# Optimization experiments

Measured on AMD Instinct MI355X. Metric: run time of the kernel, lower is better.

Reference implementation:

```python
import jax, jax.numpy as jnp
import numpy as np

N_HEAD = 16
N_EMBD = 1024
D_HEAD = N_EMBD // N_HEAD


def setup_inputs() -> dict:
    key = jax.random.key(0)
    ks = jax.random.split(key, 5)
    B, T, C = 4, 2048, N_EMBD
    s = 1.0 / np.sqrt(C)
    return {
        "x": jax.random.normal(ks[0], (B, T, C), dtype=jnp.float32),
        "w_qkv": jax.random.normal(ks[1], (C, 3 * C), dtype=jnp.float32) * s,
        "b_qkv": jnp.zeros((3 * C,), dtype=jnp.float32),
        "w_out": jax.random.normal(ks[2], (C, C), dtype=jnp.float32) * s,
        "b_out": jnp.zeros((C,), dtype=jnp.float32),
    }


def reference(x, w_qkv, b_qkv, w_out, b_out):
    B, T, C = x.shape
    qkv = x @ w_qkv + b_qkv  # [B,T,3C]
    q, k, v = jnp.split(qkv, 3, axis=-1)
    # [B,T,C] -> [B,H,T,D]
    def heads(t):
        return t.reshape(B, T, N_HEAD, D_HEAD).transpose(0, 2, 1, 3)
    q, k, v = heads(q), heads(k), heads(v)
    scores = jnp.einsum("bhqd,bhkd->bhqk", q, k) / np.sqrt(D_HEAD)
    causal = jnp.tril(jnp.ones((T, T), dtype=bool))
    scores = jnp.where(causal, scores, -jnp.inf)
    probs = jax.nn.softmax(scores, axis=-1)
    out = jnp.einsum("bhqk,bhkd->bhqd", probs, v)  # [B,H,T,D]
    out = out.transpose(0, 2, 1, 3).reshape(B, T, C)
    return out @ w_out + b_out
```

## Files before the change

### kernel.cpp

```cpp
#include <hip/hip_runtime.h>
#include <hip/hip_bf16.h>
#include <cstdint>
#include <cstddef>

typedef __attribute__((ext_vector_type(8))) short short8;
typedef __attribute__((ext_vector_type(4))) float f32x4;
typedef __attribute__((ext_vector_type(4))) uint16_t ushort4_t;

__device__ __forceinline__ uint16_t f2bf(float f) {
  union { float f; uint32_t u; } v; v.f = f;
  uint32_t r = v.u + 0x7FFFu + ((v.u >> 16) & 1u);
  return (uint16_t)(r >> 16);
}

__device__ __forceinline__ uint16_t f2bf_hw(float f) {
  union { __hip_bfloat16 h; uint16_t u; } cv;
  cv.h = __float2bfloat16(f);
  return cv.u;
}


__global__ __launch_bounds__(256) void cvt_f32_bf16(const float* __restrict__ in,
                                                    uint16_t* __restrict__ out, int n4) {
  int i = blockIdx.x * 256 + threadIdx.x;
  int stride = gridDim.x * 256;
  for (; i < n4; i += stride) {
    float4 v = ((const float4*)in)[i];
    ushort4_t o = { f2bf(v.x), f2bf(v.y), f2bf(v.z), f2bf(v.w) };
    ((ushort4_t*)out)[i] = o;
  }
}

__global__ __launch_bounds__(256) void transpose_cvt(const float* __restrict__ in,
                                                     uint16_t* __restrict__ out, int R, int C) {
  __shared__ float tile[32][33];
  int c0 = blockIdx.x * 32, r0 = blockIdx.y * 32;
  int tx = threadIdx.x, ty = threadIdx.y;
#pragma unroll
  for (int j = 0; j < 32; j += 8)
    tile[ty + j][tx] = in[(size_t)(r0 + ty + j) * C + c0 + tx];
  __syncthreads();
#pragma unroll
  for (int j = 0; j < 32; j += 8)
    out[(size_t)(c0 + ty + j) * R + r0 + tx] = f2bf(tile[tx][ty + j]);
}

__global__ __launch_bounds__(256) void transpose_v(const uint16_t* __restrict__ in,
                                                   uint16_t* __restrict__ out) {
  __shared__ uint16_t tile[32][33];
  int bh = blockIdx.z;
  int t0 = blockIdx.x * 32, d0 = blockIdx.y * 32;
  const uint16_t* ip = in + (size_t)bh * 2048 * 64;
  uint16_t* op = out + (size_t)bh * 64 * 2048;
  int tx = threadIdx.x, ty = threadIdx.y;
#pragma unroll
  for (int j = 0; j < 32; j += 8)
    tile[ty + j][tx] = ip[(size_t)(t0 + ty + j) * 64 + d0 + tx];
  __syncthreads();
#pragma unroll
  for (int j = 0; j < 32; j += 8)
    op[(size_t)(d0 + ty + j) * 2048 + t0 + tx] = tile[tx][ty + j];
}


__device__ __forceinline__ void stage16(const uint16_t* g, uint16_t* lds) {
  __builtin_amdgcn_global_load_lds((__attribute__((address_space(1))) void*)g,
                                   (__attribute__((address_space(3))) void*)lds, 16, 0, 0);
}

template <int MODE>
__global__ __launch_bounds__(256) void gemm128(
    const uint16_t* __restrict__ A, const uint16_t* __restrict__ Bt,
    const float* __restrict__ bias, int K,
    uint16_t* __restrict__ q_out, uint16_t* __restrict__ k_out, uint16_t* __restrict__ v_out,
    float* __restrict__ f_out, int N) {
  __shared__ uint16_t lA[128 * 64];
  __shared__ uint16_t lB[128 * 64];
  const int tid = threadIdx.x;
  const int lane = tid & 63;
  const int w = tid >> 6, wm = w >> 1, wn = w & 1;
  const int r16 = lane & 15, hi = lane >> 4;
  const int bn = blockIdx.x, bm = blockIdx.y;

  f32x4 acc[4][4];
#pragma unroll
  for (int i = 0; i < 4; ++i)
#pragma unroll
    for (int j = 0; j < 4; ++j) acc[i][j] = (f32x4){0.f, 0.f, 0.f, 0.f};

  const int ksteps = K >> 6;
  for (int kt = 0; kt < ksteps; ++kt) {
#pragma unroll
    for (int it = 0; it < 4; ++it) {
      int ci = it * 256 + tid;
      int row = ci >> 3;
      int cch = (ci & 7) ^ (row & 7);
      stage16(A + (size_t)(bm * 128 + row) * K + kt * 64 + cch * 8, &lA[ci * 8]);
      stage16(Bt + (size_t)(bn * 128 + row) * K + kt * 64 + cch * 8, &lB[ci * 8]);
    }
    __syncthreads();
#pragma unroll
    for (int kk = 0; kk < 2; ++kk) {
      short8 af[4], bfr[4];
      int swz = (kk * 64 + hi * 16) ^ ((r16 & 7) << 4);
#pragma unroll
      for (int i = 0; i < 4; ++i) {
        int rowa = wm * 64 + i * 16 + r16;
        af[i] = *(const short8*)((const char*)lA + rowa * 128 + swz);
        int rowb = wn * 64 + i * 16 + r16;
        bfr[i] = *(const short8*)((const char*)lB + rowb * 128 + swz);
      }
#pragma unroll
      for (int i = 0; i < 4; ++i)
#pragma unroll
        for (int j = 0; j < 4; ++j)
          acc[i][j] = __builtin_amdgcn_mfma_f32_16x16x32_bf16(af[i], bfr[j], acc[i][j], 0, 0, 0);
    }
    __syncthreads();
  }

#pragma unroll
  for (int i = 0; i < 4; ++i) {
    int rbase = bm * 128 + wm * 64 + i * 16 + hi * 4;
#pragma unroll
    for (int j = 0; j < 4; ++j) {
      int cg = bn * 128 + wn * 64 + j * 16 + r16;
      float bv = bias[cg];
      if (MODE == 0) {
        int which = cg >> 10, hh = (cg >> 6) & 15, dd = cg & 63;
        uint16_t* dst = which == 0 ? q_out : (which == 1 ? k_out : v_out);
#pragma unroll
        for (int r = 0; r < 4; ++r) {
          int rg = rbase + r;
          int bb = rg >> 11, tt = rg & 2047;
          dst[((size_t)(bb * 16 + hh) * 2048 + tt) * 64 + dd] = f2bf(acc[i][j][r] + bv);
        }
      } else {
#pragma unroll
        for (int r = 0; r < 4; ++r) {
          int rg = rbase + r;
          f_out[(size_t)rg * N + cg] = acc[i][j][r] + bv;
        }
      }
    }
  }
}

__global__ __launch_bounds__(256, 3) void attn_fwd(
    const uint16_t* __restrict__ Qm, const uint16_t* __restrict__ Km,
    const uint16_t* __restrict__ Vt, uint16_t* __restrict__ O) {
  __shared__ uint16_t kbuf[2][64 * 64];
  __shared__ uint16_t vbuf[2][64 * 64];
  __shared__ uint16_t plds[4][32 * 72];
  const int tid = threadIdx.x;
  const int lane = tid & 63, w = tid >> 6;
  const int r16 = lane & 15, hi = lane >> 4;
  const int bid = blockIdx.x;
  const int bh = (bid & 7) + 8 * ((bid >> 3) & 7);
  const int qb = 15 - (bid >> 6);
  const int b = bh >> 4, h = bh & 15;
  const size_t base = (size_t)bh * 2048 * 64;
  const int qlo = qb * 128 + w * 32;
  const int NT = 2 * qb + 2;

  const float SC = 0.18033688011112042f;
  const float BIAS = -20.197730572445487f;

  short8 ones8;
#pragma unroll
  for (int i = 0; i < 8; ++i) ones8[i] = (short)0x3F80;

  short8 aq[2][2];
#pragma unroll
  for (int st = 0; st < 2; ++st)
#pragma unroll
    for (int c = 0; c < 2; ++c)
      aq[st][c] = *(const short8*)&Qm[base + (size_t)(qlo + st * 16 + r16) * 64 + c * 32 + hi * 8];

  f32x4 o[2][4];
  f32x4 o4[2];
#pragma unroll
  for (int st = 0; st < 2; ++st) {
#pragma unroll
    for (int j = 0; j < 4; ++j) o[st][j] = (f32x4){0.f, 0.f, 0.f, 0.f};
    o4[st] = (f32x4){0.f, 0.f, 0.f, 0.f};
  }

  auto stage_tile = [&](int pb, int kv0) {
    {
      int c = tid;            int row = c >> 3, cch = (c & 7) ^ (row & 7);
      stage16(Km + base + (size_t)(kv0 + row) * 64 + cch * 8, &kbuf[pb][c * 8]);
    }
    {
      int c = tid + 256;      int row = c >> 3, cch = (c & 7) ^ (row & 7);
      stage16(Km + base + (size_t)(kv0 + row) * 64 + cch * 8, &kbuf[pb][c * 8]);
    }
    {
      int c = tid;            int row = c >> 3, cch = (c & 7) ^ (row & 7);
      stage16(Vt + base + (size_t)row * 2048 + kv0 + cch * 8, &vbuf[pb][c * 8]);
    }
    {
      int c = tid + 256;      int row = c >> 3, cch = (c & 7) ^ (row & 7);
      stage16(Vt + base + (size_t)row * 2048 + kv0 + cch * 8, &vbuf[pb][c * 8]);
    }
  };

  int pb = 0;
  stage_tile(0, 0);
#pragma unroll 1
  for (int t = 0; t < NT; ++t) {
    const int kv0 = t << 6;
    if (t + 1 < NT) {
      stage_tile(pb ^ 1, (t + 1) << 6);
      asm volatile("s_waitcnt vmcnt(4)" ::: "memory");
    } else {
      asm volatile("s_waitcnt vmcnt(0)" ::: "memory");
    }
    __builtin_amdgcn_s_barrier();
    __builtin_amdgcn_sched_barrier(0);

    if (kv0 <= qlo + 31) {
      const bool maskt = (kv0 + 64 > qlo);
      short8 bk[4][2];
#pragma unroll
      for (int ct = 0; ct < 4; ++ct)
#pragma unroll
        for (int c = 0; c < 2; ++c) {
          int row = ct * 16 + r16;
          int ch = (c * 4 + hi) ^ (row & 7);
          bk[ct][c] = *(const short8*)((const char*)&kbuf[pb][0] + row * 128 + ch * 16);
        }

#pragma unroll
      for (int st = 0; st < 2; ++st) {
        f32x4 sc[4];
#pragma unroll
        for (int ct = 0; ct < 4; ++ct) sc[ct] = (f32x4){0.f, 0.f, 0.f, 0.f};
        __builtin_amdgcn_s_setprio(1);
#pragma unroll
        for (int ct = 0; ct < 4; ++ct)
#pragma unroll
          for (int c = 0; c < 2; ++c)
            sc[ct] = __builtin_amdgcn_mfma_f32_16x16x32_bf16(bk[ct][c], aq[st][c], sc[ct], 0, 0, 0);
        __builtin_amdgcn_s_setprio(0);

        uint16_t* pl = &plds[w][st * 16 * 72];
        const int qg = qlo + st * 16 + r16;
#pragma unroll
        for (int ct = 0; ct < 4; ++ct) {
          const int kb_ = kv0 + ct * 16 + hi * 4;
          float p0 = exp2f(fmaf(sc[ct][0], SC, BIAS));
          float p1 = exp2f(fmaf(sc[ct][1], SC, BIAS));
          float p2 = exp2f(fmaf(sc[ct][2], SC, BIAS));
          float p3 = exp2f(fmaf(sc[ct][3], SC, BIAS));
          if (maskt) {
            if (kb_ + 0 > qg) p0 = 0.f;
            if (kb_ + 1 > qg) p1 = 0.f;
            if (kb_ + 2 > qg) p2 = 0.f;
            if (kb_ + 3 > qg) p3 = 0.f;
          }
          ushort4_t pk4 = { f2bf_hw(p0), f2bf_hw(p1), f2bf_hw(p2), f2bf_hw(p3) };
          *(ushort4_t*)&pl[r16 * 72 + ct * 16 + hi * 4] = pk4;
        }
      }
      asm volatile("s_waitcnt lgkmcnt(0)" ::: "memory");
      __builtin_amdgcn_sched_barrier(0);

      short8 ap[2][2];
#pragma unroll
      for (int st = 0; st < 2; ++st)
#pragma unroll
        for (int ks = 0; ks < 2; ++ks)
          ap[st][ks] = *(const short8*)&plds[w][(st * 16 + r16) * 72 + ks * 32 + hi * 8];
      short8 bv[4][2];
#pragma unroll
      for (int j = 0; j < 4; ++j)
#pragma unroll
        for (int ks = 0; ks < 2; ++ks) {
          int row = j * 16 + r16;
          int ch = (ks * 4 + hi) ^ (row & 7);
          bv[j][ks] = *(const short8*)((const char*)&vbuf[pb][0] + row * 128 + ch * 16);
        }
      __builtin_amdgcn_s_setprio(1);
#pragma unroll
      for (int st = 0; st < 2; ++st) {
#pragma unroll
        for (int ks = 0; ks < 2; ++ks)
          o4[st] = __builtin_amdgcn_mfma_f32_16x16x32_bf16(ones8, ap[st][ks], o4[st], 0, 0, 0);
#pragma unroll
        for (int j = 0; j < 4; ++j)
#pragma unroll
          for (int ks = 0; ks < 2; ++ks)
            o[st][j] = __builtin_amdgcn_mfma_f32_16x16x32_bf16(bv[j][ks], ap[st][ks], o[st][j], 0, 0, 0);
      }
      __builtin_amdgcn_s_setprio(0);
    }

    __builtin_amdgcn_s_barrier();
    __builtin_amdgcn_sched_barrier(0);
    pb ^= 1;
  }

#pragma unroll
  for (int st = 0; st < 2; ++st) {
    float inv = 1.f / o4[st][0];
    int qg = qlo + st * 16 + r16;
    size_t rowo = ((size_t)(b * 2048 + qg)) * 1024 + h * 64;
#pragma unroll
    for (int j = 0; j < 4; ++j) {
      ushort4_t v4 = { f2bf(o[st][j][0] * inv), f2bf(o[st][j][1] * inv),
                       f2bf(o[st][j][2] * inv), f2bf(o[st][j][3] * inv) };
      *(ushort4_t*)&O[rowo + j * 16 + hi * 4] = v4;
    }
  }
}


extern "C" void kernel_launch(void* const* d_in, const int* in_sizes, int n_in,
                              void* d_out, int out_size, void* d_ws, size_t ws_size,
                              hipStream_t stream) {
  const float* x = (const float*)d_in[0];
  const float* w_qkv = (const float*)d_in[1];
  const float* b_qkv = (const float*)d_in[2];
  const float* w_out = (const float*)d_in[3];
  const float* b_out = (const float*)d_in[4];
  float* out = (float*)d_out;

  const size_t BT = 8192, C = 1024, N3 = 3072, BHTD = 8388608;
  char* p = (char*)d_ws;
  uint16_t* xbf = (uint16_t*)p;   p += BT * C * 2;
  uint16_t* wqkvT = (uint16_t*)p; p += N3 * C * 2;
  uint16_t* woutT = (uint16_t*)p; p += C * C * 2;
  uint16_t* qb = (uint16_t*)p;    p += BHTD * 2;
  uint16_t* kb = (uint16_t*)p;    p += BHTD * 2;
  uint16_t* vb = (uint16_t*)p;    p += BHTD * 2;
  uint16_t* vtb = (uint16_t*)p;   p += BHTD * 2;
  uint16_t* ob = (uint16_t*)p;    p += BHTD * 2;

  cvt_f32_bf16<<<2048, 256, 0, stream>>>(x, xbf, (int)(BT * C / 4));
  transpose_cvt<<<dim3(96, 32), dim3(32, 8), 0, stream>>>(w_qkv, wqkvT, 1024, 3072);
  transpose_cvt<<<dim3(32, 32), dim3(32, 8), 0, stream>>>(w_out, woutT, 1024, 1024);
  gemm128<0><<<dim3(24, 64), 256, 0, stream>>>(xbf, wqkvT, b_qkv, 1024, qb, kb, vb, nullptr, 3072);
  transpose_v<<<dim3(64, 2, 64), dim3(32, 8), 0, stream>>>(vb, vtb);
  attn_fwd<<<1024, 256, 0, stream>>>(qb, kb, vtb, ob);
  gemm128<1><<<dim3(8, 64), 256, 0, stream>>>(ob, woutT, b_out, 1024, nullptr, nullptr, nullptr, out, 1024);
}
```

Baseline: 187.4 us.

## Use 256x256 double-buffered QKV GEMM with interleaved async staging

Replaces the 128x128 QKV projection GEMM with a dedicated 256x256-tile, 512-thread kernel. It double-buffers LDS via global_load_lds, splits each k-step into four MFMA phases interleaved with next-tile loads, and raises wave priority around the MFMAs. The launch grid is also remapped across XCDs. The larger tile cuts global traffic per FLOP and hides load latency, at the cost of 128KB of LDS and higher register pressure, which limit occupancy.

```diff
diff --git a/kernel.cpp b/kernel.cpp
--- a/kernel.cpp
+++ b/kernel.cpp
@@ -62,18 +62,154 @@
     op[(size_t)(d0 + ty + j) * 2048 + t0 + tx] = tile[tx][ty + j];
 }
 
-
 __device__ __forceinline__ void stage16(const uint16_t* g, uint16_t* lds) {
   __builtin_amdgcn_global_load_lds((__attribute__((address_space(1))) void*)g,
                                    (__attribute__((address_space(3))) void*)lds, 16, 0, 0);
 }
 
-template <int MODE>
-__global__ __launch_bounds__(256) void gemm128(
+__global__ __launch_bounds__(512, 2) void gemm256_qkv(
     const uint16_t* __restrict__ A, const uint16_t* __restrict__ Bt,
-    const float* __restrict__ bias, int K,
-    uint16_t* __restrict__ q_out, uint16_t* __restrict__ k_out, uint16_t* __restrict__ v_out,
-    float* __restrict__ f_out, int N) {
+    const float* __restrict__ bias,
+    uint16_t* __restrict__ q_out, uint16_t* __restrict__ k_out, uint16_t* __restrict__ v_out) {
+  constexpr int K = 1024, KT = 16;
+  __shared__ uint16_t lA[2][2][8192];
+  __shared__ uint16_t lB[2][2][8192];
+  const int tid = threadIdx.x;
+  const int lane = tid & 63, w = tid >> 6;
+  const int wm = w >> 2, wn = w & 3;
+  const int r16 = lane & 15, hi = lane >> 4;
+  const int wgid = (blockIdx.x & 7) * 48 + (blockIdx.x >> 3);
+  const int bn = wgid % 12, bm = wgid / 12;
+
+  const int row0 = tid >> 3;
+  const int cch0 = (tid & 7) ^ (row0 & 7);
+  const uint16_t* aS = A + ((size_t)bm * 256 + row0) * K + cch0 * 8;
+  const uint16_t* bS = Bt + ((size_t)bn * 256 + row0) * K + cch0 * 8;
+
+  f32x4 acc[8][4];
+#pragma unroll
+  for (int m = 0; m < 8; ++m)
+#pragma unroll
+    for (int n = 0; n < 4; ++n) acc[m][n] = (f32x4){0.f, 0.f, 0.f, 0.f};
+
+  auto stA = [&](int pn, int h, int ktn) {
+    stage16(aS + (size_t)(h * 128) * K + ktn * 64, &lA[pn][h][tid * 8]);
+    stage16(aS + (size_t)(h * 128 + 64) * K + ktn * 64, &lA[pn][h][4096 + tid * 8]);
+  };
+  auto stB = [&](int pn, int h, int ktn) {
+    stage16(bS + (size_t)(h * 128) * K + ktn * 64, &lB[pn][h][tid * 8]);
+    stage16(bS + (size_t)(h * 128 + 64) * K + ktn * 64, &lB[pn][h][4096 + tid * 8]);
+  };
+
+  stA(0, 0, 0); stA(0, 1, 0); stB(0, 0, 0); stB(0, 1, 0);
+
+#pragma unroll 1
+  for (int kt = 0; kt < KT; ++kt) {
+    const int p = kt & 1;
+    if (kt + 1 < KT) {
+      stA(p ^ 1, 0, kt + 1);
+      asm volatile("s_waitcnt vmcnt(2)" ::: "memory");
+    } else {
+      asm volatile("s_waitcnt vmcnt(0)" ::: "memory");
+    }
+    __builtin_amdgcn_s_barrier();
+    __builtin_amdgcn_sched_barrier(0);
+
+    const char* lap = (const char*)&lA[p][wm][0];
+    const char* lbp = (const char*)&lB[p][wn >> 1][0];
+    short8 af[4], bfr[4];
+
+#pragma unroll
+    for (int n = 0; n < 4; ++n) {
+      int rowb = (wn & 1) * 64 + n * 16 + r16;
+      bfr[n] = *(const short8*)(lbp + rowb * 128 + ((hi ^ (rowb & 7)) << 4));
+    }
+#pragma unroll
+    for (int mm = 0; mm < 4; ++mm) {
+      int rowa = mm * 16 + r16;
+      af[mm] = *(const short8*)(lap + rowa * 128 + ((hi ^ (rowa & 7)) << 4));
+    }
+    __builtin_amdgcn_s_setprio(1);
+#pragma unroll
+    for (int mm = 0; mm < 4; ++mm)
+#pragma unroll
+      for (int n = 0; n < 4; ++n)
+        acc[mm][n] = __builtin_amdgcn_mfma_f32_16x16x32_bf16(af[mm], bfr[n], acc[mm][n], 0, 0, 0);
+    __builtin_amdgcn_s_setprio(0);
+    if (kt + 1 < KT) stA(p ^ 1, 1, kt + 1);
+
+#pragma unroll
+    for (int mm = 0; mm < 4; ++mm) {
+      int rowa = 64 + mm * 16 + r16;
+      af[mm] = *(const short8*)(lap + rowa * 128 + ((hi ^ (rowa & 7)) << 4));
+    }
+    __builtin_amdgcn_s_setprio(1);
+#pragma unroll
+    for (int mm = 0; mm < 4; ++mm)
+#pragma unroll
+      for (int n = 0; n < 4; ++n)
+        acc[4 + mm][n] = __builtin_amdgcn_mfma_f32_16x16x32_bf16(af[mm], bfr[n], acc[4 + mm][n], 0, 0, 0);
+    __builtin_amdgcn_s_setprio(0);
+    if (kt + 1 < KT) stB(p ^ 1, 0, kt + 1);
+
+#pragma unroll
+    for (int n = 0; n < 4; ++n) {
+      int rowb = (wn & 1) * 64 + n * 16 + r16;
+      bfr[n] = *(const short8*)(lbp + rowb * 128 + (((4 + hi) ^ (rowb & 7)) << 4));
+    }
+#pragma unroll
+    for (int mm = 0; mm < 4; ++mm) {
+      int rowa = mm * 16 + r16;
+      af[mm] = *(const short8*)(lap + rowa * 128 + (((4 + hi) ^ (rowa & 7)) << 4));
+    }
+    __builtin_amdgcn_s_setprio(1);
+#pragma unroll
+    for (int mm = 0; mm < 4; ++mm)
+#pragma unroll
+      for (int n = 0; n < 4; ++n)
+        acc[mm][n] = __builtin_amdgcn_mfma_f32_16x16x32_bf16(af[mm], bfr[n], acc[mm][n], 0, 0, 0);
+    __builtin_amdgcn_s_setprio(0);
+    if (kt + 1 < KT) stB(p ^ 1, 1, kt + 1);
+
+#pragma unroll
+    for (int mm = 0; mm < 4; ++mm) {
+      int rowa = 64 + mm * 16 + r16;
+      af[mm] = *(const short8*)(lap + rowa * 128 + (((4 + hi) ^ (rowa & 7)) << 4));
+    }
+    __builtin_amdgcn_s_setprio(1);
+#pragma unroll
+    for (int mm = 0; mm < 4; ++mm)
+#pragma unroll
+      for (int n = 0; n < 4; ++n)
+        acc[4 + mm][n] = __builtin_amdgcn_mfma_f32_16x16x32_bf16(af[mm], bfr[n], acc[4 + mm][n], 0, 0, 0);
+    __builtin_amdgcn_s_setprio(0);
+
+    __builtin_amdgcn_s_barrier();
+    __builtin_amdgcn_sched_barrier(0);
+  }
+
+#pragma unroll
+  for (int m = 0; m < 8; ++m) {
+    int rg = bm * 256 + wm * 128 + m * 16 + hi * 4;
+#pragma unroll
+    for (int n = 0; n < 4; ++n) {
+      int cg = bn * 256 + wn * 64 + n * 16 + r16;
+      float bv = bias[cg];
+      int which = cg >> 10, hh = (cg >> 6) & 15, dd = cg & 63;
+      uint16_t* dst = which == 0 ? q_out : (which == 1 ? k_out : v_out);
+#pragma unroll
+      for (int r = 0; r < 4; ++r) {
+        int rgr = rg + r;
+        dst[((size_t)((rgr >> 11) * 16 + hh) * 2048 + (rgr & 2047)) * 64 + dd] = f2bf(acc[m][n][r] + bv);
+      }
+    }
+  }
+}
+
+
+__global__ __launch_bounds__(256) void gemm128_out(
+    const uint16_t* __restrict__ A, const uint16_t* __restrict__ Bt,
+    const float* __restrict__ bias, int K, float* __restrict__ f_out, int N) {
   __shared__ uint16_t lA[128 * 64];
   __shared__ uint16_t lB[128 * 64];
   const int tid = threadIdx.x;
@@ -126,22 +262,9 @@
     for (int j = 0; j < 4; ++j) {
       int cg = bn * 128 + wn * 64 + j * 16 + r16;
       float bv = bias[cg];
-      if (MODE == 0) {
-        int which = cg >> 10, hh = (cg >> 6) & 15, dd = cg & 63;
-        uint16_t* dst = which == 0 ? q_out : (which == 1 ? k_out : v_out);
-#pragma unroll
-        for (int r = 0; r < 4; ++r) {
-          int rg = rbase + r;
-          int bb = rg >> 11, tt = rg & 2047;
-          dst[((size_t)(bb * 16 + hh) * 2048 + tt) * 64 + dd] = f2bf(acc[i][j][r] + bv);
-        }
-      } else {
-#pragma unroll
-        for (int r = 0; r < 4; ++r) {
-          int rg = rbase + r;
-          f_out[(size_t)rg * N + cg] = acc[i][j][r] + bv;
-        }
-      }
+#pragma unroll
+      for (int r = 0; r < 4; ++r)
+        f_out[(size_t)(rbase + r) * N + cg] = acc[i][j][r] + bv;
     }
   }
 }
@@ -340,8 +463,8 @@
   cvt_f32_bf16<<<2048, 256, 0, stream>>>(x, xbf, (int)(BT * C / 4));
   transpose_cvt<<<dim3(96, 32), dim3(32, 8), 0, stream>>>(w_qkv, wqkvT, 1024, 3072);
   transpose_cvt<<<dim3(32, 32), dim3(32, 8), 0, stream>>>(w_out, woutT, 1024, 1024);
-  gemm128<0><<<dim3(24, 64), 256, 0, stream>>>(xbf, wqkvT, b_qkv, 1024, qb, kb, vb, nullptr, 3072);
+  gemm256_qkv<<<384, 512, 0, stream>>>(xbf, wqkvT, b_qkv, qb, kb, vb);
   transpose_v<<<dim3(64, 2, 64), dim3(32, 8), 0, stream>>>(vb, vtb);
   attn_fwd<<<1024, 256, 0, stream>>>(qb, kb, vtb, ob);
-  gemm128<1><<<dim3(8, 64), 256, 0, stream>>>(ob, woutT, b_out, 1024, nullptr, nullptr, nullptr, out, 1024);
-}
+  gemm128_out<<<dim3(8, 64), 256, 0, stream>>>(ob, woutT, b_out, 1024, out, 1024);
+}
```

After: 199.0 us. 1.06x slower.

## Use 256x128 tiles with swizzled block order for the QKV projection GEMM

Applied to the files above, without the earlier changes.

Splits the templated GEMM into a dedicated QKV kernel with a 256x128 output tile (8x4 MFMA accumulators per wave), a compile-time K, an XCD-aware remapping of the block index, and raised MFMA issue priority. The larger M tile halves B-tile reloads per output and improves LDS-to-MFMA reuse. The grid remap is meant to improve L2 locality across chiplets. In exchange it uses more registers and 48KB of LDS per block, which may limit occupancy, and the output GEMM keeps the old tiling.

```diff
diff --git a/kernel.cpp b/kernel.cpp
--- a/kernel.cpp
+++ b/kernel.cpp
@@ -62,18 +62,98 @@
     op[(size_t)(d0 + ty + j) * 2048 + t0 + tx] = tile[tx][ty + j];
 }
 
-
 __device__ __forceinline__ void stage16(const uint16_t* g, uint16_t* lds) {
   __builtin_amdgcn_global_load_lds((__attribute__((address_space(1))) void*)g,
                                    (__attribute__((address_space(3))) void*)lds, 16, 0, 0);
 }
 
-template <int MODE>
-__global__ __launch_bounds__(256) void gemm128(
+__global__ __launch_bounds__(256, 3) void gemm_qkv(
     const uint16_t* __restrict__ A, const uint16_t* __restrict__ Bt,
-    const float* __restrict__ bias, int K,
-    uint16_t* __restrict__ q_out, uint16_t* __restrict__ k_out, uint16_t* __restrict__ v_out,
-    float* __restrict__ f_out, int N) {
+    const float* __restrict__ bias,
+    uint16_t* __restrict__ q_out, uint16_t* __restrict__ k_out, uint16_t* __restrict__ v_out) {
+  constexpr int K = 1024, KT = 16;
+  __shared__ uint16_t lA[256 * 64];
+  __shared__ uint16_t lB[128 * 64];
+  const int tid = threadIdx.x;
+  const int lane = tid & 63, w = tid >> 6;
+  const int wm = w >> 1, wn = w & 1;
+  const int r16 = lane & 15, hi = lane >> 4;
+  const int wg = (blockIdx.x & 7) * 96 + (blockIdx.x >> 3);
+  const int bm = wg / 24, bn = wg % 24;
+
+  const int row0 = tid >> 3;
+  const int cch0 = (tid & 7) ^ (row0 & 7);
+  const uint16_t* aS = A + ((size_t)bm * 256 + row0) * K + cch0 * 8;
+  const uint16_t* bS = Bt + ((size_t)bn * 128 + row0) * K + cch0 * 8;
+
+  f32x4 acc[8][4];
+#pragma unroll
+  for (int m = 0; m < 8; ++m)
+#pragma unroll
+    for (int n = 0; n < 4; ++n) acc[m][n] = (f32x4){0.f, 0.f, 0.f, 0.f};
+
+#pragma unroll 1
+  for (int kt = 0; kt < KT; ++kt) {
+#pragma unroll
+    for (int it = 0; it < 8; ++it)
+      stage16(aS + (size_t)(it * 32) * K + kt * 64, &lA[it * 2048 + tid * 8]);
+#pragma unroll
+    for (int it = 0; it < 4; ++it)
+      stage16(bS + (size_t)(it * 32) * K + kt * 64, &lB[it * 2048 + tid * 8]);
+    __syncthreads();
+
+#pragma unroll
+    for (int kk = 0; kk < 2; ++kk) {
+      short8 bfr[4];
+      const int swz = (kk * 64 + hi * 16) ^ ((r16 & 7) << 4);
+#pragma unroll
+      for (int n = 0; n < 4; ++n) {
+        int rowb = wn * 64 + n * 16 + r16;
+        bfr[n] = *(const short8*)((const char*)lB + rowb * 128 + swz);
+      }
+#pragma unroll
+      for (int mh = 0; mh < 2; ++mh) {
+        short8 af[4];
+#pragma unroll
+        for (int i = 0; i < 4; ++i) {
+          int rowa = wm * 128 + mh * 64 + i * 16 + r16;
+          af[i] = *(const short8*)((const char*)lA + rowa * 128 + swz);
+        }
+        __builtin_amdgcn_s_setprio(1);
+#pragma unroll
+        for (int i = 0; i < 4; ++i)
+#pragma unroll
+          for (int n = 0; n < 4; ++n)
+            acc[mh * 4 + i][n] =
+                __builtin_amdgcn_mfma_f32_16x16x32_bf16(af[i], bfr[n], acc[mh * 4 + i][n], 0, 0, 0);
+        __builtin_amdgcn_s_setprio(0);
+      }
+    }
+    __syncthreads();
+  }
+
+#pragma unroll
+  for (int m = 0; m < 8; ++m) {
+    int rg = bm * 256 + wm * 128 + (m >> 2) * 64 + (m & 3) * 16 + hi * 4;
+#pragma unroll
+    for (int n = 0; n < 4; ++n) {
+      int cg = bn * 128 + wn * 64 + n * 16 + r16;
+      float bv = bias[cg];
+      int which = cg >> 10, hh = (cg >> 6) & 15, dd = cg & 63;
+      uint16_t* dst = which == 0 ? q_out : (which == 1 ? k_out : v_out);
+#pragma unroll
+      for (int r = 0; r < 4; ++r) {
+        int rgr = rg + r;
+        dst[((size_t)((rgr >> 11) * 16 + hh) * 2048 + (rgr & 2047)) * 64 + dd] = f2bf(acc[m][n][r] + bv);
+      }
+    }
+  }
+}
+
+
+__global__ __launch_bounds__(256) void gemm128_out(
+    const uint16_t* __restrict__ A, const uint16_t* __restrict__ Bt,
+    const float* __restrict__ bias, int K, float* __restrict__ f_out, int N) {
   __shared__ uint16_t lA[128 * 64];
   __shared__ uint16_t lB[128 * 64];
   const int tid = threadIdx.x;
@@ -126,22 +206,9 @@
     for (int j = 0; j < 4; ++j) {
       int cg = bn * 128 + wn * 64 + j * 16 + r16;
       float bv = bias[cg];
-      if (MODE == 0) {
-        int which = cg >> 10, hh = (cg >> 6) & 15, dd = cg & 63;
-        uint16_t* dst = which == 0 ? q_out : (which == 1 ? k_out : v_out);
-#pragma unroll
-        for (int r = 0; r < 4; ++r) {
-          int rg = rbase + r;
-          int bb = rg >> 11, tt = rg & 2047;
-          dst[((size_t)(bb * 16 + hh) * 2048 + tt) * 64 + dd] = f2bf(acc[i][j][r] + bv);
-        }
-      } else {
-#pragma unroll
-        for (int r = 0; r < 4; ++r) {
-          int rg = rbase + r;
-          f_out[(size_t)rg * N + cg] = acc[i][j][r] + bv;
-        }
-      }
+#pragma unroll
+      for (int r = 0; r < 4; ++r)
+        f_out[(size_t)(rbase + r) * N + cg] = acc[i][j][r] + bv;
     }
   }
 }
@@ -340,8 +407,8 @@
   cvt_f32_bf16<<<2048, 256, 0, stream>>>(x, xbf, (int)(BT * C / 4));
   transpose_cvt<<<dim3(96, 32), dim3(32, 8), 0, stream>>>(w_qkv, wqkvT, 1024, 3072);
   transpose_cvt<<<dim3(32, 32), dim3(32, 8), 0, stream>>>(w_out, woutT, 1024, 1024);
-  gemm128<0><<<dim3(24, 64), 256, 0, stream>>>(xbf, wqkvT, b_qkv, 1024, qb, kb, vb, nullptr, 3072);
+  gemm_qkv<<<768, 256, 0, stream>>>(xbf, wqkvT, b_qkv, qb, kb, vb);
   transpose_v<<<dim3(64, 2, 64), dim3(32, 8), 0, stream>>>(vb, vtb);
   attn_fwd<<<1024, 256, 0, stream>>>(qb, kb, vtb, ob);
-  gemm128<1><<<dim3(8, 64), 256, 0, stream>>>(ob, woutT, b_out, 1024, nullptr, nullptr, nullptr, out, 1024);
-}
+  gemm128_out<<<dim3(8, 64), 256, 0, stream>>>(ob, woutT, b_out, 1024, out, 1024);
+}
```

Measured after the change: 182.8 us. 2.4% less time.
